# Kernel tuning notes

Hardware: AMD Instinct MI355X
Metric: run time of the kernel (lower is better)

Reference implementation:

```python
import jax, jax.numpy as jnp
import numpy as np

B, N, H = 128, 1024, 128          # graphs, nodes per graph, hidden size
K1, K2, K3 = 512, 256, 128        # ceil(ratio^l * N), ratio = 0.5
DEG = 8                           # avg degree
E = B * N * DEG                   # total edges (fixed, masked after pooling)


def gcn_conv(x, row, col, mask, W, b, n):
    h = x @ W
    deg = jax.ops.segment_sum(mask, col, num_segments=n) + 1.0  # + self loop
    dinv = jax.lax.rsqrt(deg)
    coef = (dinv[row] * dinv[col] * mask)[:, None]
    agg = jax.ops.segment_sum(h[row] * coef, col, num_segments=n)
    return agg + h * (dinv * dinv)[:, None] + b  # self-loop term + bias


def topk_pool(x, row, col, mask, p, n_graphs, n_per, k):
    # PyG TopKPooling: y = x.p/||p||, keep per-graph top-k, x' = x[perm]*tanh(y[perm])
    score = (x @ p) / jnp.linalg.norm(p)
    vals, idx = jax.lax.top_k(score.reshape(n_graphs, n_per), k)  # [B, k]
    sel = (idx + (jnp.arange(n_graphs) * n_per)[:, None]).reshape(-1)
    xs = x[sel] * jnp.tanh(vals.reshape(-1))[:, None]
    # relabel edges; drop edges touching removed nodes via mask
    newid = jnp.full((n_graphs * n_per,), -1, jnp.int32).at[sel].set(
        jnp.arange(n_graphs * k, dtype=jnp.int32))
    nr, nc = newid[row], newid[col]
    nmask = mask * ((nr >= 0) & (nc >= 0)).astype(mask.dtype)
    return xs, jnp.maximum(nr, 0), jnp.maximum(nc, 0), nmask


def readout(x, n_graphs, k):
    # cat([gmp, gap]) with contiguous equal-size graphs
    xg = x.reshape(n_graphs, k, -1)
    return jnp.concatenate([xg.max(axis=1), xg.mean(axis=1)], axis=1)


def _forward(x, edge_row, edge_col, W1, b1, p1, W2, b2, p2, W3, b3, p3):
    mask = jnp.ones((E,), x.dtype)
    h = jax.nn.relu(gcn_conv(x, edge_row, edge_col, mask, W1, b1, B * N))
    x1, r, c, m = topk_pool(h, edge_row, edge_col, mask, p1, B, N, K1)
    out = readout(x1, B, K1)
    h = jax.nn.relu(gcn_conv(x1, r, c, m, W2, b2, B * K1))
    x2, r, c, m = topk_pool(h, r, c, m, p2, B, K1, K2)
    out = out + readout(x2, B, K2)
    h = jax.nn.relu(gcn_conv(x2, r, c, m, W3, b3, B * K2))
    x3, r, c, m = topk_pool(h, r, c, m, p3, B, K2, K3)
    out = out + readout(x3, B, K3)
    return out  # [B, 2*H]


def setup_inputs() -> dict:
    key = jax.random.key(0)
    ks = jax.random.split(key, 12)
    x = jax.random.normal(ks[0], (B * N, H), jnp.float32)
    off = (jnp.arange(B, dtype=jnp.int32) * N)[:, None]
    edge_row = (jax.random.randint(ks[1], (B, N * DEG), 0, N, jnp.int32) + off).reshape(-1)
    edge_col = (jax.random.randint(ks[2], (B, N * DEG), 0, N, jnp.int32) + off).reshape(-1)
    s = 1.0 / np.sqrt(H)
    params = {}
    for i, tag in enumerate(["1", "2", "3"]):
        params["W" + tag] = jax.random.normal(ks[3 + 3 * i], (H, H), jnp.float32) * s
        params["b" + tag] = jnp.zeros((H,), jnp.float32)
        params["p" + tag] = jax.random.normal(ks[4 + 3 * i], (H,), jnp.float32)
    return {"x": x, "edge_row": edge_row, "edge_col": edge_col, **params}


def reference(x, edge_row, edge_col, W1, b1, p1, W2, b2, p2, W3, b3, p3):
    return _forward(x, edge_row, edge_col, W1, b1, p1, W2, b2, p2, W3, b3, p3)
```

## Files before the change

kernel.cpp:

```cpp
#include <hip/hip_runtime.h>
#include <math.h>

#define BG   128
#define NPER 1024
#define HDIM 128
#define NEDGE (BG * NPER * 8)
#define NMAX (BG * NPER)
#define EPG  (NEDGE / BG)
#define CAP  48
#define PRE  16

typedef __attribute__((ext_vector_type(8))) short s16x8;
typedef __attribute__((ext_vector_type(4))) float f32x4;

static __device__ __forceinline__ ushort f2bf(float f) {
  uint u = __float_as_uint(f);
  return (ushort)((u + 0x7fffu + ((u >> 16) & 1u)) >> 16);
}
static __device__ __forceinline__ float bf2f(ushort h) {
  return __uint_as_float(((uint)h) << 16);
}


__global__ __launch_bounds__(256) void countfill_kernel(
    const int* __restrict__ cr, const int* __restrict__ cc,
    int* __restrict__ cnt, int* __restrict__ meta8,
    int* __restrict__ srcext, int mask) {
  int e = blockIdx.x * 256 + threadIdx.x;
  int c = cc[e];
  int rl = cr[e] & mask;
  int pos = atomicAdd(&cnt[c], 1);
  if (pos < PRE) {
    meta8[(size_t)c * PRE + pos] = rl;
  } else if (pos < CAP) {
    srcext[(size_t)c * CAP + pos] = rl;
  }
}


__global__ __launch_bounds__(1024) void degorder_kernel(
    const int* __restrict__ cnt, int* __restrict__ order,
    int* __restrict__ odeg) {
  __shared__ int bb[2];
  int g = blockIdx.x, t = threadIdx.x;
  if (t < 2) bb[t] = 0;
  __syncthreads();
  int d = cnt[g * NPER + t];
  int bkt = d > 8 ? 1 : 0;
  int pos = atomicAdd(&bb[bkt], 1);
  __syncthreads();
  int slot = bkt ? bb[0] + pos : pos;
  order[g * NPER + slot] = t;
  odeg[g * NPER + slot] = d;
}

extern __shared__ float ldsbuf[];


__global__ __launch_bounds__(1024) void agg_lds_kernel(
    const float* __restrict__ x, float* __restrict__ z,
    const int* __restrict__ meta8, const int* __restrict__ srcext,
    const int* __restrict__ deg, const int* __restrict__ order,
    const int* __restrict__ odeg, int npg) {
  float* sX = ldsbuf;
  float* sDinv = sX + npg * 32;
  int g = blockIdx.x >> 2;
  int chunk = blockIdx.x & 3;
  int t = threadIdx.x;
  int base = g * npg;

  const float4* x4 = (const float4*)x;
  float4* sX4 = (float4*)sX;
  for (int i = t; i < npg * 8; i += 1024) {
    int r = i >> 3, l8 = i & 7;
    float dv = rsqrtf((float)deg[base + r] + 1.0f);
    float4 v = x4[(size_t)(base + r) * 32 + chunk * 8 + l8];
    v.x *= dv; v.y *= dv; v.z *= dv; v.w *= dv;
    sX4[i] = v;
  }
  for (int i = t; i < npg; i += 1024)
    sDinv[i] = rsqrtf((float)deg[base + i] + 1.0f);

  int dl = t >> 3, l = t & 7;
  const int4* m4 = (const int4*)meta8;
  float4* z4 = (float4*)z;

  int ordc = order[base + dl];
  int dpc  = odeg[base + dl];
  int ordn = order[base + dl + 128];
  int dpn  = odeg[base + dl + 128];
  int4 c0 = m4[(size_t)(base + ordc) * 4 + 0];
  int4 c1 = m4[(size_t)(base + ordc) * 4 + 1];
  int4 c2 = {0, 0, 0, 0}, c3 = {0, 0, 0, 0};
  if (dpc > 8) {
    c2 = m4[(size_t)(base + ordc) * 4 + 2];
    c3 = m4[(size_t)(base + ordc) * 4 + 3];
  }

  __syncthreads();

  for (int slot = dl; slot < npg; slot += 128) {
    int ordn2 = ordn, dpn2 = dpn;
    if (slot + 256 < npg) {
      ordn2 = order[base + slot + 256];
      dpn2  = odeg[base + slot + 256];
    }
    int4 n0 = {0,0,0,0}, n1 = {0,0,0,0}, n2 = {0,0,0,0}, n3 = {0,0,0,0};
    if (slot + 128 < npg) {
      n0 = m4[(size_t)(base + ordn) * 4 + 0];
      n1 = m4[(size_t)(base + ordn) * 4 + 1];
      if (dpn > 8) {
        n2 = m4[(size_t)(base + ordn) * 4 + 2];
        n3 = m4[(size_t)(base + ordn) * 4 + 3];
      }
    }

    int dst = ordc;
    int node = base + dst;
    int d = dpc > CAP ? CAP : dpc;
    int dp = d > PRE ? PRE : d;
    float dc = sDinv[dst];

    int sA0 = (0 < dp) ? c0.x : dst;
    int sA1 = (1 < dp) ? c0.y : dst;
    int sA2 = (2 < dp) ? c0.z : dst;
    int sA3 = (3 < dp) ? c0.w : dst;
    int sA4 = (4 < dp) ? c1.x : dst;
    int sA5 = (5 < dp) ? c1.y : dst;
    int sA6 = (6 < dp) ? c1.z : dst;
    int sA7 = (7 < dp) ? c1.w : dst;
    float4 w  = sX4[dst * 8 + l];
    float4 p0 = sX4[sA0 * 8 + l];
    float4 p1 = sX4[sA1 * 8 + l];
    float4 p2 = sX4[sA2 * 8 + l];
    float4 p3 = sX4[sA3 * 8 + l];
    float4 p4 = sX4[sA4 * 8 + l];
    float4 p5 = sX4[sA5 * 8 + l];
    float4 p6 = sX4[sA6 * 8 + l];
    float4 p7 = sX4[sA7 * 8 + l];
    float4 a0, a1, a2, a3;
    a0.x = w.x + p0.x; a0.y = w.y + p0.y; a0.z = w.z + p0.z; a0.w = w.w + p0.w;
    a1.x = p1.x + p5.x; a1.y = p1.y + p5.y; a1.z = p1.z + p5.z; a1.w = p1.w + p5.w;
    a2.x = p2.x + p6.x; a2.y = p2.y + p6.y; a2.z = p2.z + p6.z; a2.w = p2.w + p6.w;
    a3.x = p3.x + p7.x; a3.y = p3.y + p7.y; a3.z = p3.z + p7.z; a3.w = p3.w + p7.w;
    a0.x += p4.x; a0.y += p4.y; a0.z += p4.z; a0.w += p4.w;

    int nslots = 8;
    if (dp > 8) {
      int sB0 = (8 < dp)  ? c2.x : dst;
      int sB1 = (9 < dp)  ? c2.y : dst;
      int sB2 = (10 < dp) ? c2.z : dst;
      int sB3 = (11 < dp) ? c2.w : dst;
      int sB4 = (12 < dp) ? c3.x : dst;
      int sB5 = (13 < dp) ? c3.y : dst;
      int sB6 = (14 < dp) ? c3.z : dst;
      int sB7 = (15 < dp) ? c3.w : dst;
      float4 q0 = sX4[sB0 * 8 + l];
      float4 q1 = sX4[sB1 * 8 + l];
      float4 q2 = sX4[sB2 * 8 + l];
      float4 q3 = sX4[sB3 * 8 + l];
      float4 q4 = sX4[sB4 * 8 + l];
      float4 q5 = sX4[sB5 * 8 + l];
      float4 q6 = sX4[sB6 * 8 + l];
      float4 q7 = sX4[sB7 * 8 + l];
      a0.x += q0.x; a0.y += q0.y; a0.z += q0.z; a0.w += q0.w;
      a1.x += q1.x; a1.y += q1.y; a1.z += q1.z; a1.w += q1.w;
      a2.x += q2.x; a2.y += q2.y; a2.z += q2.z; a2.w += q2.w;
      a3.x += q3.x; a3.y += q3.y; a3.z += q3.z; a3.w += q3.w;
      a0.x += q4.x; a0.y += q4.y; a0.z += q4.z; a0.w += q4.w;
      a1.x += q5.x; a1.y += q5.y; a1.z += q5.z; a1.w += q5.w;
      a2.x += q6.x; a2.y += q6.y; a2.z += q6.z; a2.w += q6.w;
      a3.x += q7.x; a3.y += q7.y; a3.z += q7.z; a3.w += q7.w;
      nslots = 16;
    }

    if (d > PRE) {
      for (int e2 = PRE; e2 < d; ++e2) {
        int rl = srcext[(size_t)node * CAP + e2];
        float4 v0 = sX4[rl * 8 + l];
        a0.x += v0.x; a0.y += v0.y; a0.z += v0.z; a0.w += v0.w;
      }
    }

    float corr = (float)(nslots - dp);
    float4 o;
    o.x = (a0.x + a1.x + a2.x + a3.x - corr * w.x) * dc;
    o.y = (a0.y + a1.y + a2.y + a3.y - corr * w.y) * dc;
    o.z = (a0.z + a1.z + a2.z + a3.z - corr * w.z) * dc;
    o.w = (a0.w + a1.w + a2.w + a3.w - corr * w.w) * dc;
    z4[(size_t)node * 32 + chunk * 8 + l] = o;

    ordc = ordn; dpc = dpn; ordn = ordn2; dpn = dpn2;
    c0 = n0; c1 = n1; c2 = n2; c3 = n3;
  }
}


__global__ __launch_bounds__(256) void wsplit_kernel(
    const float* __restrict__ W0, const float* __restrict__ W1,
    const float* __restrict__ W2, ushort* __restrict__ wpk) {
  int id = blockIdx.x * 256 + threadIdx.x;
  int L = id >> 14;
  int r = id & 16383;
  int i = r & 7;
  int lane = (r >> 3) & 63;
  int nt = (r >> 9) & 7;
  int kt = (r >> 12) & 3;
  int k = kt * 32 + (lane >> 4) * 8 + i;
  int n = nt * 16 + (lane & 15);
  const float* W = (L == 0) ? W0 : (L == 1) ? W1 : W2;
  float v = W[k * HDIM + n];
  ushort h = f2bf(v);
  float r1 = v - bf2f(h);
  ushort m = f2bf(r1);
  ushort lo = f2bf(r1 - bf2f(m));
  size_t base = (size_t)L * 3 * 16384 + (size_t)r;
  wpk[base] = h;
  wpk[base + 16384] = m;
  wpk[base + 32768] = lo;
}


__global__ __launch_bounds__(256, 2) void conv_mfma_kernel(
    float* __restrict__ zh, const ushort* __restrict__ wpk,
    const float* __restrict__ bias, const float* __restrict__ p,
    float* __restrict__ score) {
  int t = threadIdx.x;
  int wv = t >> 6, l = t & 63;
  int lr = l & 15, lq = l >> 4;
  int arowA = blockIdx.x * 128 + wv * 16 + lr;
  int arowB = arowA + 64;
  const float* zrowA = zh + (size_t)arowA * HDIM + lq * 8;
  const float* zrowB = zh + (size_t)arowB * HDIM + lq * 8;

  s16x8 ahA[4], amA[4], alA[4], ahB[4], amB[4], alB[4];
  #pragma unroll
  for (int kt = 0; kt < 4; ++kt) {
    float4 v0 = ((const float4*)(zrowA + kt * 32))[0];
    float4 v1 = ((const float4*)(zrowA + kt * 32))[1];
    float fA[8] = {v0.x, v0.y, v0.z, v0.w, v1.x, v1.y, v1.z, v1.w};
    float4 u0 = ((const float4*)(zrowB + kt * 32))[0];
    float4 u1 = ((const float4*)(zrowB + kt * 32))[1];
    float fB[8] = {u0.x, u0.y, u0.z, u0.w, u1.x, u1.y, u1.z, u1.w};
    #pragma unroll
    for (int i = 0; i < 8; ++i) {
      ushort h = f2bf(fA[i]);
      float r1 = fA[i] - bf2f(h);
      ushort m = f2bf(r1);
      ushort lo = f2bf(r1 - bf2f(m));
      ahA[kt][i] = (short)h; amA[kt][i] = (short)m; alA[kt][i] = (short)lo;
      h = f2bf(fB[i]);
      r1 = fB[i] - bf2f(h);
      m = f2bf(r1);
      lo = f2bf(r1 - bf2f(m));
      ahB[kt][i] = (short)h; amB[kt][i] = (short)m; alB[kt][i] = (short)lo;
    }
  }

  f32x4 accA[8], accB[8];
  #pragma unroll
  for (int nt = 0; nt < 8; ++nt) { accA[nt] = (f32x4)(0.f); accB[nt] = (f32x4)(0.f); }

  const s16x8* wh = (const s16x8*)wpk;
  const s16x8* wm = wh + 2048;
  const s16x8* wl = wm + 2048;

  #pragma unroll
  for (int kt = 0; kt < 4; ++kt) {
    #pragma unroll
    for (int nt = 0; nt < 8; ++nt) {
      int fi = (kt * 8 + nt) * 64 + l;
      s16x8 bh = wh[fi];
      s16x8 bm = wm[fi];
      s16x8 bl = wl[fi];
      accA[nt] = __builtin_amdgcn_mfma_f32_16x16x32_bf16(ahA[kt], bh, accA[nt], 0, 0, 0);
      accA[nt] = __builtin_amdgcn_mfma_f32_16x16x32_bf16(ahA[kt], bm, accA[nt], 0, 0, 0);
      accA[nt] = __builtin_amdgcn_mfma_f32_16x16x32_bf16(amA[kt], bh, accA[nt], 0, 0, 0);
      accA[nt] = __builtin_amdgcn_mfma_f32_16x16x32_bf16(ahA[kt], bl, accA[nt], 0, 0, 0);
      accA[nt] = __builtin_amdgcn_mfma_f32_16x16x32_bf16(alA[kt], bh, accA[nt], 0, 0, 0);
      accA[nt] = __builtin_amdgcn_mfma_f32_16x16x32_bf16(amA[kt], bm, accA[nt], 0, 0, 0);
      accB[nt] = __builtin_amdgcn_mfma_f32_16x16x32_bf16(ahB[kt], bh, accB[nt], 0, 0, 0);
      accB[nt] = __builtin_amdgcn_mfma_f32_16x16x32_bf16(ahB[kt], bm, accB[nt], 0, 0, 0);
      accB[nt] = __builtin_amdgcn_mfma_f32_16x16x32_bf16(amB[kt], bh, accB[nt], 0, 0, 0);
      accB[nt] = __builtin_amdgcn_mfma_f32_16x16x32_bf16(ahB[kt], bl, accB[nt], 0, 0, 0);
      accB[nt] = __builtin_amdgcn_mfma_f32_16x16x32_bf16(alB[kt], bh, accB[nt], 0, 0, 0);
      accB[nt] = __builtin_amdgcn_mfma_f32_16x16x32_bf16(amB[kt], bm, accB[nt], 0, 0, 0);
    }
  }

  int orowA = blockIdx.x * 128 + wv * 16 + lq * 4;
  int orowB = orowA + 64;
  float partA[4] = {0.f, 0.f, 0.f, 0.f};
  float partB[4] = {0.f, 0.f, 0.f, 0.f};
  #pragma unroll
  for (int nt = 0; nt < 8; ++nt) {
    float bv = bias[nt * 16 + lr];
    float pv = p[nt * 16 + lr];
    #pragma unroll
    for (int j = 0; j < 4; ++j) {
      float hA = fmaxf(accA[nt][j] + bv, 0.f);
      partA[j] += hA * pv;
      zh[(size_t)(orowA + j) * HDIM + nt * 16 + lr] = hA;
      float hB = fmaxf(accB[nt][j] + bv, 0.f);
      partB[j] += hB * pv;
      zh[(size_t)(orowB + j) * HDIM + nt * 16 + lr] = hB;
    }
  }
  #pragma unroll
  for (int j = 0; j < 4; ++j) {
    #pragma unroll
    for (int s = 1; s < 16; s <<= 1) {
      partA[j] += __shfl_xor(partA[j], s);
      partB[j] += __shfl_xor(partB[j], s);
    }
    if (lr == 0) {
      score[orowA + j] = partA[j];
      score[orowB + j] = partB[j];
    }
  }
}


__global__ __launch_bounds__(1024) void topk_mega_kernel(
    const float* __restrict__ score, const float* __restrict__ p,
    const float* __restrict__ h, float* __restrict__ xo,
    const int* __restrict__ in_r, const int* __restrict__ in_c,
    int* __restrict__ out_r, int* __restrict__ out_c,
    int* __restrict__ meta8, int* __restrict__ srcext,
    int* __restrict__ cnt, float* __restrict__ acc,
    int* __restrict__ order, int* __restrict__ odeg,
    float* __restrict__ outf, int P, int K, int L) {
  __shared__ float sv[1024];
  __shared__ int si[1024];
  __shared__ int snew[1024];
  __shared__ int scnt[512];
  __shared__ int bb[2];
  __shared__ float s_pn;
  __shared__ float4 smx[32][32], ssm[32][32];
  int g = blockIdx.x;
  int t = threadIdx.x;

  if (L < 2 && t < 512) scnt[t] = 0;
  if (t < 2) bb[t] = 0;
  snew[t] = -1;
  if (t < 128) { float v = p[t]; sv[t] = v * v; }
  __syncthreads();
  for (int off = 64; off; off >>= 1) {
    if (t < off) sv[t] += sv[t + off];
    __syncthreads();
  }
  if (t == 0) s_pn = sqrtf(sv[0]);
  __syncthreads();
  float pn = s_pn;

  sv[t] = score[(size_t)g * P + t];
  si[t] = t;
  for (int size = 2; size <= P; size <<= 1) {
    for (int stride = size >> 1; stride; stride >>= 1) {
      __syncthreads();
      int j = t ^ stride;
      if (j > t) {
        float a = sv[t], b = sv[j];
        int ia = si[t], ib = si[j];
        bool tFirst = (a > b) || (a == b && ia < ib);
        bool up = ((t & size) == 0);
        if (up ? !tFirst : tFirst) {
          sv[t] = b; sv[j] = a;
          si[t] = ib; si[j] = ia;
        }
      }
    }
  }
  __syncthreads();
  if (t < K) {
    snew[si[t]] = t;
    sv[t] = tanhf(sv[t] / pn);
  }
  __syncthreads();

  int lane = t & 31, grp = t >> 5;
  const float4* h4 = (const float4*)h;
  float4* xo4 = (float4*)xo;
  size_t hbase = (size_t)g * P * 32;
  float4 mx = make_float4(-INFINITY, -INFINITY, -INFINITY, -INFINITY);
  float4 sm = make_float4(0.f, 0.f, 0.f, 0.f);
  #pragma unroll
  for (int i = 0; i < 16; ++i) {
    int j = grp * 16 + i;
    float th = sv[j];
    float4 v = h4[hbase + (size_t)si[j] * 32 + lane];
    v.x *= th; v.y *= th; v.z *= th; v.w *= th;
    xo4[((size_t)g * K + j) * 32 + lane] = v;
    mx.x = fmaxf(mx.x, v.x); mx.y = fmaxf(mx.y, v.y);
    mx.z = fmaxf(mx.z, v.z); mx.w = fmaxf(mx.w, v.w);
    sm.x += v.x; sm.y += v.y; sm.z += v.z; sm.w += v.w;
  }
  smx[grp][lane] = mx;
  ssm[grp][lane] = sm;
  __syncthreads();
  int ngrp = P >> 5;
  if (grp == 0) {
    for (int s2 = 1; s2 < ngrp; ++s2) {
      float4 m2 = smx[s2][lane], s3 = ssm[s2][lane];
      mx.x = fmaxf(mx.x, m2.x); mx.y = fmaxf(mx.y, m2.y);
      mx.z = fmaxf(mx.z, m2.z); mx.w = fmaxf(mx.w, m2.w);
      sm.x += s3.x; sm.y += s3.y; sm.z += s3.z; sm.w += s3.w;
    }
    int c0 = lane * 4;
    if (L < 2) {
      float* amax = acc + (size_t)L * BG * 256 + (size_t)g * 256;
      float* asum = amax + 128;
      amax[c0 + 0] = mx.x; amax[c0 + 1] = mx.y;
      amax[c0 + 2] = mx.z; amax[c0 + 3] = mx.w;
      asum[c0 + 0] = sm.x; asum[c0 + 1] = sm.y;
      asum[c0 + 2] = sm.z; asum[c0 + 3] = sm.w;
    } else {
      sv[c0 + 0] = mx.x; sv[c0 + 1] = mx.y;
      sv[c0 + 2] = mx.z; sv[c0 + 3] = mx.w;
      sv[128 + c0 + 0] = sm.x; sv[128 + c0 + 1] = sm.y;
      sv[128 + c0 + 2] = sm.z; sv[128 + c0 + 3] = sm.w;
    }
  }

  if (L == 2) {
    __syncthreads();
    float v;
    const float* a0 = acc + (size_t)g * 256;
    const float* a1 = acc + (size_t)BG * 256 + (size_t)g * 256;
    if (t < 128) {
      v = a0[t] + a1[t] + sv[t];
    } else {
      v = a0[t] * (1.f / 512.f) + a1[t] * (1.f / 256.f) + sv[t] * (1.f / 128.f);
    }
    outf[g * 256 + t] = v;
    return;
  }

  int ept = EPG / P;
  int ebase = g * EPG;
  for (int i = 0; i < ept; ++i) {
    int e = ebase + i * P + t;
    int r = in_r[e];
    int nr = -1, nc = -1;
    if (r >= 0) {
      nr = snew[r & (P - 1)];
      nc = snew[in_c[e] & (P - 1)];
    }
    bool ok = (nr >= 0) && (nc >= 0);
    out_r[e] = ok ? g * K + nr : -1;
    out_c[e] = ok ? g * K + nc : -1;
    if (ok) {
      int pos = atomicAdd(&scnt[nc], 1);
      size_t gnode = (size_t)g * K + nc;
      if (pos < PRE) {
        meta8[gnode * PRE + pos] = nr;
      } else if (pos < CAP) {
        srcext[gnode * CAP + pos] = nr;
      }
    }
  }
  __syncthreads();
  if (t < K) cnt[g * K + t] = scnt[t];

  int bkt = 0, bpos = 0, bdeg = 0;
  if (t < K) {
    bdeg = scnt[t];
    bkt = bdeg > 8 ? 1 : 0;
    bpos = atomicAdd(&bb[bkt], 1);
  }
  __syncthreads();
  if (t < K) {
    int slot = bkt ? bb[0] + bpos : bpos;
    order[g * K + slot] = t;
    odeg[g * K + slot] = bdeg;
  }
}


extern "C" void kernel_launch(void* const* d_in, const int* in_sizes, int n_in,
                              void* d_out, int out_size, void* d_ws, size_t ws_size,
                              hipStream_t stream) {
  const float* x0 = (const float*)d_in[0];
  const int* erow = (const int*)d_in[1];
  const int* ecol = (const int*)d_in[2];
  const float* Wm[3] = {(const float*)d_in[3], (const float*)d_in[6], (const float*)d_in[9]};
  const float* bm[3] = {(const float*)d_in[4], (const float*)d_in[7], (const float*)d_in[10]};
  const float* pm[3] = {(const float*)d_in[5], (const float*)d_in[8], (const float*)d_in[11]};

  char* w = (char*)d_ws;
  size_t off = 0;
  auto alloc = [&](size_t bytes) -> void* {
    void* ptr = w + off;
    off = (off + bytes + 255) & ~(size_t)255;
    return ptr;
  };
  int* cur_row = (int*)alloc((size_t)NEDGE * 4);
  int* cur_col = (int*)alloc((size_t)NEDGE * 4);
  int* meta8   = (int*)alloc((size_t)NMAX * PRE * 4);
  int* srcext  = (int*)alloc((size_t)NMAX * CAP * 4);
  int* cnt     = (int*)alloc((size_t)NMAX * 4);
  int* order   = (int*)alloc((size_t)NMAX * 4);
  int* odeg    = (int*)alloc((size_t)NMAX * 4);
  float* score = (float*)alloc((size_t)NMAX * 4);
  float* acc   = (float*)alloc((size_t)2 * BG * 256 * 4);
  float* zh    = (float*)alloc((size_t)NMAX * HDIM * 4);
  float* x1    = (float*)alloc((size_t)BG * 512 * HDIM * 4);
  float* x2    = (float*)alloc((size_t)BG * 256 * HDIM * 4);
  float* x3    = (float*)alloc((size_t)BG * 128 * HDIM * 4);
  ushort* wpk  = (ushort*)alloc((size_t)3 * 3 * 16384 * 2);

  hipFuncSetAttribute((const void*)agg_lds_kernel,
                      hipFuncAttributeMaxDynamicSharedMemorySize, 152 * 1024);

  hipMemsetAsync(cnt, 0, (size_t)NMAX * 4, stream);
  countfill_kernel<<<NEDGE / 256, 256, 0, stream>>>(erow, ecol, cnt, meta8,
                                                    srcext, NPER - 1);
  wsplit_kernel<<<(3 * 16384) / 256, 256, 0, stream>>>(Wm[0], Wm[1], Wm[2], wpk);
  degorder_kernel<<<BG, 1024, 0, stream>>>(cnt, order, odeg);

  const float* xin = x0;
  float* xout[3] = {x1, x2, x3};
  int Ps[3] = {1024, 512, 256};

  for (int L = 0; L < 3; ++L) {
    int P = Ps[L];
    int K = P >> 1;
    int n = BG * P;
    const int* in_r = (L == 0) ? erow : cur_row;
    const int* in_c = (L == 0) ? ecol : cur_col;
    size_t ldsBytes = (size_t)(P * 33) * 4;

    agg_lds_kernel<<<BG * 4, 1024, ldsBytes, stream>>>(
        xin, zh, meta8, srcext, cnt, order, odeg, P);
    conv_mfma_kernel<<<n / 128, 256, 0, stream>>>(
        zh, wpk + (size_t)L * 3 * 16384, bm[L], pm[L], score);
    topk_mega_kernel<<<BG, P, 0, stream>>>(
        score, pm[L], zh, xout[L], in_r, in_c, cur_row, cur_col,
        meta8, srcext, cnt, acc, order, odeg, (float*)d_out, P, K, L);
    xin = xout[L];
  }
}
```

Before: 369.4 us.

## Fuse edge count/fill and degree ordering into one per-graph LDS kernel

Replaces the global-atomic count/fill kernel, the cnt memset, and the degree-ordering kernel with one kernel per graph. It bins edges by destination using LDS atomics and stages the first 16 sources in LDS before writing them out coalesced. Global atomics and two launches are removed. Only 128 blocks run, which may underuse the GPU, and the kernel relies on each graph's edges being contiguous and within the graph.

```diff
diff --git a/kernel.cpp b/kernel.cpp
--- a/kernel.cpp
+++ b/kernel.cpp
@@ -21,40 +21,62 @@
   return __uint_as_float(((uint)h) << 16);
 }
 
-
-__global__ __launch_bounds__(256) void countfill_kernel(
+extern __shared__ float ldsbuf[];
+
+
+__global__ __launch_bounds__(1024) void countfill_lds_kernel(
     const int* __restrict__ cr, const int* __restrict__ cc,
     int* __restrict__ cnt, int* __restrict__ meta8,
-    int* __restrict__ srcext, int mask) {
-  int e = blockIdx.x * 256 + threadIdx.x;
-  int c = cc[e];
-  int rl = cr[e] & mask;
-  int pos = atomicAdd(&cnt[c], 1);
-  if (pos < PRE) {
-    meta8[(size_t)c * PRE + pos] = rl;
-  } else if (pos < CAP) {
-    srcext[(size_t)c * CAP + pos] = rl;
-  }
-}
-
-
-__global__ __launch_bounds__(1024) void degorder_kernel(
-    const int* __restrict__ cnt, int* __restrict__ order,
+    int* __restrict__ srcext, int* __restrict__ order,
     int* __restrict__ odeg) {
-  __shared__ int bb[2];
+  int* smeta = (int*)ldsbuf;
+  int* scnt  = smeta + NPER * PRE;
+  int* sbb   = scnt + NPER;
   int g = blockIdx.x, t = threadIdx.x;
-  if (t < 2) bb[t] = 0;
-  __syncthreads();
-  int d = cnt[g * NPER + t];
+  scnt[t] = 0;
+  if (t < 2) sbb[t] = 0;
+  __syncthreads();
+
+  const int4* cr4 = (const int4*)(cr + (size_t)g * EPG);
+  const int4* cc4 = (const int4*)(cc + (size_t)g * EPG);
+  #pragma unroll
+  for (int i = 0; i < 2; ++i) {
+    int4 r = cr4[t * 2 + i];
+    int4 c = cc4[t * 2 + i];
+    int rl, cl, pos;
+    cl = c.x & (NPER - 1); rl = r.x & (NPER - 1);
+    pos = atomicAdd(&scnt[cl], 1);
+    if (pos < PRE) smeta[cl * PRE + pos] = rl;
+    else if (pos < CAP) srcext[((size_t)g * NPER + cl) * CAP + pos] = rl;
+    cl = c.y & (NPER - 1); rl = r.y & (NPER - 1);
+    pos = atomicAdd(&scnt[cl], 1);
+    if (pos < PRE) smeta[cl * PRE + pos] = rl;
+    else if (pos < CAP) srcext[((size_t)g * NPER + cl) * CAP + pos] = rl;
+    cl = c.z & (NPER - 1); rl = r.z & (NPER - 1);
+    pos = atomicAdd(&scnt[cl], 1);
+    if (pos < PRE) smeta[cl * PRE + pos] = rl;
+    else if (pos < CAP) srcext[((size_t)g * NPER + cl) * CAP + pos] = rl;
+    cl = c.w & (NPER - 1); rl = r.w & (NPER - 1);
+    pos = atomicAdd(&scnt[cl], 1);
+    if (pos < PRE) smeta[cl * PRE + pos] = rl;
+    else if (pos < CAP) srcext[((size_t)g * NPER + cl) * CAP + pos] = rl;
+  }
+  __syncthreads();
+
+  int4* mo = (int4*)(meta8 + (size_t)g * NPER * PRE);
+  const int4* sm4 = (const int4*)smeta;
+  #pragma unroll
+  for (int i = 0; i < 4; ++i) mo[i * 1024 + t] = sm4[i * 1024 + t];
+  int d = scnt[t];
+  cnt[g * NPER + t] = d;
+
   int bkt = d > 8 ? 1 : 0;
-  int pos = atomicAdd(&bb[bkt], 1);
-  __syncthreads();
-  int slot = bkt ? bb[0] + pos : pos;
+  int bpos = atomicAdd(&sbb[bkt], 1);
+  __syncthreads();
+  int slot = bkt ? sbb[0] + bpos : bpos;
   order[g * NPER + slot] = t;
   odeg[g * NPER + slot] = d;
 }
-
-extern __shared__ float ldsbuf[];
 
 
 __global__ __launch_bounds__(1024) void agg_lds_kernel(
@@ -511,12 +533,13 @@
 
   hipFuncSetAttribute((const void*)agg_lds_kernel,
                       hipFuncAttributeMaxDynamicSharedMemorySize, 152 * 1024);
-
-  hipMemsetAsync(cnt, 0, (size_t)NMAX * 4, stream);
-  countfill_kernel<<<NEDGE / 256, 256, 0, stream>>>(erow, ecol, cnt, meta8,
-                                                    srcext, NPER - 1);
+  hipFuncSetAttribute((const void*)countfill_lds_kernel,
+                      hipFuncAttributeMaxDynamicSharedMemorySize, 72 * 1024);
+
+  size_t cfLds = (size_t)(NPER * PRE + NPER + 2) * 4;
+  countfill_lds_kernel<<<BG, 1024, cfLds, stream>>>(
+      erow, ecol, cnt, meta8, srcext, order, odeg);
   wsplit_kernel<<<(3 * 16384) / 256, 256, 0, stream>>>(Wm[0], Wm[1], Wm[2], wpk);
-  degorder_kernel<<<BG, 1024, 0, stream>>>(cnt, order, odeg);
 
   const float* xin = x0;
   float* xout[3] = {x1, x2, x3};
```

After: 327.1 us. 1.13x faster.
